# Kernel optimization log

Measured on AMD Instinct MI355X. Metric: run time of the kernel, lower is better.

## Reference

```python
import jax, jax.numpy as jnp
import numpy as np

DT = 0.01
MIN_VARIANCE = 0.01
REG_WEIGHT = 0.01
EPS = 1e-06


def setup_inputs() -> dict:
    key = jax.random.key(0)
    k1, k2, k3, k4 = jax.random.split(key, 4)
    B, T = 256, 16384
    return {
        "vel_pred": jax.random.normal(k1, (B, T, 2), dtype=jnp.float32),
        "cov_pred": jax.random.normal(k2, (B, T, 2), dtype=jnp.float32),
        "vel_gt": jax.random.normal(k3, (B, T, 2), dtype=jnp.float32),
        "pos_gt": jax.random.normal(k4, (B, T, 2), dtype=jnp.float32),
        "log_delta_v": jnp.zeros((), dtype=jnp.float32),
        "log_delta_c": jnp.zeros((), dtype=jnp.float32),
    }


def reference(vel_pred, cov_pred, vel_gt, pos_gt, log_delta_v, log_delta_c):
    # Sequential loop pos[t] = pos[t-1] + vel_pred[t-1]*dt, pos[0] = vel_pred[0]*dt
    # == dt * (vel_pred[:, 0:1] + exclusive_cumsum_T(vel_pred))  -- a parallel scan.
    excl = jnp.concatenate(
        [jnp.zeros_like(vel_pred[:, :1]), jnp.cumsum(vel_pred[:, :-1], axis=1)], axis=1
    )
    pos_pred = (vel_pred[:, :1] + excl) * DT  # [B, T, 2]

    lv_p = jnp.mean((pos_pred - pos_gt) ** 2)
    lv_e = jnp.mean((vel_pred - vel_gt) ** 2)
    lv_total = lv_p + lv_e

    sigma = jnp.clip(jnp.exp(cov_pred), MIN_VARIANCE, None)  # [B, T, 2] diag cov
    inv_sigma = 1.0 / sigma
    diff = vel_gt - vel_pred
    mahal = jnp.sum(inv_sigma * diff ** 2, axis=-1)  # [B, T]
    log_det = jnp.log(sigma[..., 0] * sigma[..., 1] + EPS)
    lc_total = 0.5 * jnp.mean(mahal + log_det)

    delta_v = jnp.exp(log_delta_v)
    delta_c = jnp.exp(log_delta_c)
    total_loss = (
        lv_total / (2.0 * delta_v ** 2)
        + lc_total / (2.0 * delta_c ** 2)
        + log_delta_v
        + log_delta_c
    )
    reg = jnp.mean(jnp.sum(inv_sigma, axis=-1))
    total_loss = total_loss + REG_WEIGHT * reg
    return total_loss
```

## Files before the change

kernel.cpp:

```cpp
#include <hip/hip_runtime.h>

static constexpr int B_ = 256;
static constexpr int T_ = 16384;
static constexpr int TPB = 1024;
static constexpr int F4_ROW = T_ * 2 / 4;
static constexpr int F4_THR = F4_ROW / TPB;

static constexpr float DTc    = 0.01f;
static constexpr float MINVAR = 0.01f;
static constexpr float EPSc   = 1e-6f;


__device__ __forceinline__ float waveReduce(float v) {
#pragma unroll
  for (int d = 32; d > 0; d >>= 1) v += __shfl_down(v, d, 64);
  return v;
}
__device__ __forceinline__ double waveReduceD(double v) {
#pragma unroll
  for (int d = 32; d > 0; d >>= 1) v += __shfl_down(v, d, 64);
  return v;
}

__global__ __launch_bounds__(TPB) void fusedKern(
    const float4* __restrict__ vel, const float4* __restrict__ cov,
    const float4* __restrict__ vgt, const float4* __restrict__ pgt,
    float* __restrict__ pPos, float* __restrict__ pLve,
    float* __restrict__ pLc,  float* __restrict__ pReg) {
  const int b = blockIdx.x;
  const int tid = threadIdx.x;
  const int lane = tid & 63, wid = tid >> 6;
  const int tbase = b * F4_ROW + tid * F4_THR;

  float4 v[F4_THR];
#pragma unroll
  for (int j = 0; j < F4_THR; ++j) v[j] = vel[tbase + j];

  float ex[F4_THR], ey[F4_THR];
  float vx[F4_THR], vy[F4_THR];
  float tx = 0.f, ty = 0.f;
#pragma unroll
  for (int j = 0; j < F4_THR; ++j) {
    ex[j] = tx; ey[j] = ty;
    vx[j] = v[j].x; vy[j] = v[j].y;
    tx += v[j].x + v[j].z;
    ty += v[j].y + v[j].w;
  }

  float lve = 0.f, lc = 0.f, reg = 0.f;
#pragma unroll
  for (int j = 0; j < F4_THR; ++j) {
    float4 c = cov[tbase + j];
    float4 g = vgt[tbase + j];
    {
      float dx = g.x - v[j].x, dy = g.y - v[j].y;
      float sqx = dx * dx, sqy = dy * dy;
      lve += sqx + sqy;
      float sx = fmaxf(__expf(c.x), MINVAR);
      float sy = fmaxf(__expf(c.y), MINVAR);
      float ixv = 1.0f / sx, iyv = 1.0f / sy;
      lc += ixv * sqx + iyv * sqy + __logf(sx * sy + EPSc);
      reg += ixv + iyv;
    }
    {
      float dx = g.z - v[j].z, dy = g.w - v[j].w;
      float sqx = dx * dx, sqy = dy * dy;
      lve += sqx + sqy;
      float sx = fmaxf(__expf(c.z), MINVAR);
      float sy = fmaxf(__expf(c.w), MINVAR);
      float ixv = 1.0f / sx, iyv = 1.0f / sy;
      lc += ixv * sqx + iyv * sqy + __logf(sx * sy + EPSc);
      reg += ixv + iyv;
    }
  }

  float sx = tx, sy = ty;
#pragma unroll
  for (int d = 1; d < 64; d <<= 1) {
    float ux = __shfl_up(sx, (unsigned)d, 64);
    float uy = __shfl_up(sy, (unsigned)d, 64);
    if (lane >= d) { sx += ux; sy += uy; }
  }
  const float wxx = sx - tx, wxy = sy - ty;

  __shared__ float2 wt[16];
  __shared__ float  sh[4][16];
  if (lane == 63) wt[wid] = make_float2(sx, sy);
  __syncthreads();

  float ax = (lane < 16) ? wt[lane].x : 0.f;
  float ay = (lane < 16) ? wt[lane].y : 0.f;
  float iax = ax, iay = ay;
#pragma unroll
  for (int d = 1; d < 16; d <<= 1) {
    float ux = __shfl_up(iax, (unsigned)d, 64);
    float uy = __shfl_up(iay, (unsigned)d, 64);
    if (lane >= d) { iax += ux; iay += uy; }
  }
  const float bx0 = __shfl(iax - ax, wid, 64);
  const float by0 = __shfl(iay - ay, wid, 64);

  const float2 v0 = ((const float2*)vel)[b * T_];

  float apos = 0.f;
#pragma unroll
  for (int j = 0; j < F4_THR; ++j) {
    float4 q = pgt[tbase + j];
    float px0 = bx0 + wxx + ex[j];
    float py0 = by0 + wxy + ey[j];
    float px = DTc * (v0.x + px0), py = DTc * (v0.y + py0);
    float e0 = px - q.x, e1 = py - q.y;
    apos += e0 * e0 + e1 * e1;
    px = DTc * (v0.x + px0 + vx[j]); py = DTc * (v0.y + py0 + vy[j]);
    e0 = px - q.z; e1 = py - q.w;
    apos += e0 * e0 + e1 * e1;
  }

  float r0 = waveReduce(apos);
  float r1 = waveReduce(lve);
  float r2 = waveReduce(lc);
  float r3 = waveReduce(reg);
  if (lane == 0) { sh[0][wid] = r0; sh[1][wid] = r1; sh[2][wid] = r2; sh[3][wid] = r3; }
  __syncthreads();
  if (tid == 0) {
    float t0 = 0.f, t1 = 0.f, t2 = 0.f, t3 = 0.f;
#pragma unroll
    for (int w = 0; w < 16; ++w) { t0 += sh[0][w]; t1 += sh[1][w]; t2 += sh[2][w]; t3 += sh[3][w]; }
    pPos[b] = t0; pLve[b] = t1; pLc[b] = t2; pReg[b] = t3;
  }
}

__global__ __launch_bounds__(256) void kernC(
    const float* __restrict__ pPos, const float* __restrict__ pLve,
    const float* __restrict__ pLc,  const float* __restrict__ pReg,
    const float* __restrict__ pldv, const float* __restrict__ pldc,
    float* __restrict__ out) {
  const int tid = threadIdx.x;
  const int lane = tid & 63, wid = tid >> 6;
  double a0 = (double)pPos[tid];
  double a1 = (double)pLve[tid];
  double a2 = (double)pLc[tid];
  double a3 = (double)pReg[tid];
  a0 = waveReduceD(a0);
  a1 = waveReduceD(a1);
  a2 = waveReduceD(a2);
  a3 = waveReduceD(a3);
  __shared__ double sh[4][4];
  if (lane == 0) { sh[0][wid] = a0; sh[1][wid] = a1; sh[2][wid] = a2; sh[3][wid] = a3; }
  __syncthreads();
  if (tid == 0) {
    double pos_sq = sh[0][0] + sh[0][1] + sh[0][2] + sh[0][3];
    double vel_sq = sh[1][0] + sh[1][1] + sh[1][2] + sh[1][3];
    double lcs    = sh[2][0] + sh[2][1] + sh[2][2] + sh[2][3];
    double regs   = sh[3][0] + sh[3][1] + sh[3][2] + sh[3][3];
    const double NBT2 = (double)B_ * (double)T_ * 2.0;
    const double NBT  = (double)B_ * (double)T_;
    double lv  = (pos_sq + vel_sq) / NBT2;
    double lc  = 0.5 * lcs / NBT;
    double reg = regs / NBT;
    double ldv = (double)pldv[0], ldc = (double)pldc[0];
    double total = lv / (2.0 * exp(2.0 * ldv)) + lc / (2.0 * exp(2.0 * ldc))
                 + ldv + ldc + 0.01 * reg;
    out[0] = (float)total;
  }
}

extern "C" void kernel_launch(void* const* d_in, const int* in_sizes, int n_in,
                              void* d_out, int out_size, void* d_ws, size_t ws_size,
                              hipStream_t stream) {
  const float4* vel = (const float4*)d_in[0];
  const float4* cov = (const float4*)d_in[1];
  const float4* vgt = (const float4*)d_in[2];
  const float4* pgt = (const float4*)d_in[3];
  const float* ldv = (const float*)d_in[4];
  const float* ldc = (const float*)d_in[5];

  char* ws = (char*)d_ws;
  float* pPos = (float*)ws;
  float* pLve = (float*)(ws + 1024);
  float* pLc  = (float*)(ws + 2048);
  float* pReg = (float*)(ws + 3072);

  fusedKern<<<B_, TPB, 0, stream>>>(vel, cov, vgt, pgt, pPos, pLve, pLc, pReg);
  kernC<<<1, 256, 0, stream>>>(pPos, pLve, pLc, pReg, ldv, ldc, (float*)d_out);
}
```

Before: 166.0 us.

## Split each row into segments and fix up the position loss algebraically

Each row of the time dimension is split into 8 segments, each handled by its own 256-thread block, so the launch grows from 256 to 2048 blocks for better occupancy and latency hiding. The prefix offset between segments is not known inside a block, so each block stores the sum of squared errors plus their linear sums. The second kernel then rebuilds the exact squared error from these using the expansion (e+dt*C)^2. All four input loads are also issued up front to raise memory-level parallelism. The cost is more registers per thread, a larger finalize step, and float cancellation risk in the algebraic correction.

```diff
diff --git a/kernel.cpp b/kernel.cpp
--- a/kernel.cpp
+++ b/kernel.cpp
@@ -2,9 +2,13 @@
 
 static constexpr int B_ = 256;
 static constexpr int T_ = 16384;
-static constexpr int TPB = 1024;
+static constexpr int THREADS = 256;
+static constexpr int SEG_T = 2048;
+static constexpr int NSEG = T_ / SEG_T;
+static constexpr int NBLK = B_ * NSEG;
 static constexpr int F4_ROW = T_ * 2 / 4;
-static constexpr int F4_THR = F4_ROW / TPB;
+static constexpr int F4_SEG = SEG_T * 2 / 4;
+static constexpr int F4_THR = F4_SEG / THREADS;
 
 static constexpr float DTc    = 0.01f;
 static constexpr float MINVAR = 0.01f;
@@ -22,56 +26,35 @@
   return v;
 }
 
-__global__ __launch_bounds__(TPB) void fusedKern(
+__global__ __launch_bounds__(THREADS) void kern1(
     const float4* __restrict__ vel, const float4* __restrict__ cov,
     const float4* __restrict__ vgt, const float4* __restrict__ pgt,
-    float* __restrict__ pPos, float* __restrict__ pLve,
-    float* __restrict__ pLc,  float* __restrict__ pReg) {
-  const int b = blockIdx.x;
+    float2* __restrict__ segsum, float* __restrict__ se2,
+    float* __restrict__ sex, float* __restrict__ sey,
+    float* __restrict__ pLve, float* __restrict__ pLc, float* __restrict__ pReg) {
+  const int bid = blockIdx.x;
+  const int b = bid >> 3, s = bid & (NSEG - 1);
   const int tid = threadIdx.x;
   const int lane = tid & 63, wid = tid >> 6;
-  const int tbase = b * F4_ROW + tid * F4_THR;
-
-  float4 v[F4_THR];
+  const int tbase = b * F4_ROW + s * F4_SEG + tid * F4_THR;
+
+  float4 v[F4_THR], c[F4_THR], g[F4_THR], q[F4_THR];
 #pragma unroll
   for (int j = 0; j < F4_THR; ++j) v[j] = vel[tbase + j];
+#pragma unroll
+  for (int j = 0; j < F4_THR; ++j) c[j] = cov[tbase + j];
+#pragma unroll
+  for (int j = 0; j < F4_THR; ++j) g[j] = vgt[tbase + j];
+#pragma unroll
+  for (int j = 0; j < F4_THR; ++j) q[j] = pgt[tbase + j];
 
   float ex[F4_THR], ey[F4_THR];
-  float vx[F4_THR], vy[F4_THR];
   float tx = 0.f, ty = 0.f;
 #pragma unroll
   for (int j = 0; j < F4_THR; ++j) {
     ex[j] = tx; ey[j] = ty;
-    vx[j] = v[j].x; vy[j] = v[j].y;
     tx += v[j].x + v[j].z;
     ty += v[j].y + v[j].w;
-  }
-
-  float lve = 0.f, lc = 0.f, reg = 0.f;
-#pragma unroll
-  for (int j = 0; j < F4_THR; ++j) {
-    float4 c = cov[tbase + j];
-    float4 g = vgt[tbase + j];
-    {
-      float dx = g.x - v[j].x, dy = g.y - v[j].y;
-      float sqx = dx * dx, sqy = dy * dy;
-      lve += sqx + sqy;
-      float sx = fmaxf(__expf(c.x), MINVAR);
-      float sy = fmaxf(__expf(c.y), MINVAR);
-      float ixv = 1.0f / sx, iyv = 1.0f / sy;
-      lc += ixv * sqx + iyv * sqy + __logf(sx * sy + EPSc);
-      reg += ixv + iyv;
-    }
-    {
-      float dx = g.z - v[j].z, dy = g.w - v[j].w;
-      float sqx = dx * dx, sqy = dy * dy;
-      lve += sqx + sqy;
-      float sx = fmaxf(__expf(c.z), MINVAR);
-      float sy = fmaxf(__expf(c.w), MINVAR);
-      float ixv = 1.0f / sx, iyv = 1.0f / sy;
-      lc += ixv * sqx + iyv * sqy + __logf(sx * sy + EPSc);
-      reg += ixv + iyv;
-    }
   }
 
   float sx = tx, sy = ty;
@@ -81,72 +64,114 @@
     float uy = __shfl_up(sy, (unsigned)d, 64);
     if (lane >= d) { sx += ux; sy += uy; }
   }
-  const float wxx = sx - tx, wxy = sy - ty;
-
-  __shared__ float2 wt[16];
-  __shared__ float  sh[4][16];
+  const float wexx = sx - tx, wexy = sy - ty;
+
+  __shared__ float2 wt[4];
   if (lane == 63) wt[wid] = make_float2(sx, sy);
   __syncthreads();
 
-  float ax = (lane < 16) ? wt[lane].x : 0.f;
-  float ay = (lane < 16) ? wt[lane].y : 0.f;
-  float iax = ax, iay = ay;
-#pragma unroll
-  for (int d = 1; d < 16; d <<= 1) {
-    float ux = __shfl_up(iax, (unsigned)d, 64);
-    float uy = __shfl_up(iay, (unsigned)d, 64);
-    if (lane >= d) { iax += ux; iay += uy; }
-  }
-  const float bx0 = __shfl(iax - ax, wid, 64);
-  const float by0 = __shfl(iay - ay, wid, 64);
+  float offx = wexx, offy = wexy;
+  float segx = 0.f, segy = 0.f;
+#pragma unroll
+  for (int w = 0; w < 4; ++w) {
+    float2 t = wt[w];
+    if (w < wid) { offx += t.x; offy += t.y; }
+    segx += t.x; segy += t.y;
+  }
 
   const float2 v0 = ((const float2*)vel)[b * T_];
 
-  float apos = 0.f;
+  float ase2 = 0.f, asex = 0.f, asey = 0.f;
 #pragma unroll
   for (int j = 0; j < F4_THR; ++j) {
-    float4 q = pgt[tbase + j];
-    float px0 = bx0 + wxx + ex[j];
-    float py0 = by0 + wxy + ey[j];
-    float px = DTc * (v0.x + px0), py = DTc * (v0.y + py0);
-    float e0 = px - q.x, e1 = py - q.y;
-    apos += e0 * e0 + e1 * e1;
-    px = DTc * (v0.x + px0 + vx[j]); py = DTc * (v0.y + py0 + vy[j]);
-    e0 = px - q.z; e1 = py - q.w;
-    apos += e0 * e0 + e1 * e1;
-  }
-
-  float r0 = waveReduce(apos);
-  float r1 = waveReduce(lve);
-  float r2 = waveReduce(lc);
-  float r3 = waveReduce(reg);
-  if (lane == 0) { sh[0][wid] = r0; sh[1][wid] = r1; sh[2][wid] = r2; sh[3][wid] = r3; }
+    float px0 = offx + ex[j], py0 = offy + ey[j];
+    float e0x = DTc * (v0.x + px0) - q[j].x;
+    float e0y = DTc * (v0.y + py0) - q[j].y;
+    float e1x = DTc * (v0.x + px0 + v[j].x) - q[j].z;
+    float e1y = DTc * (v0.y + py0 + v[j].y) - q[j].w;
+    ase2 += e0x * e0x + e0y * e0y + e1x * e1x + e1y * e1y;
+    asex += e0x + e1x;
+    asey += e0y + e1y;
+  }
+
+  float lve = 0.f, lc = 0.f, reg = 0.f;
+#pragma unroll
+  for (int j = 0; j < F4_THR; ++j) {
+    {
+      float dx = g[j].x - v[j].x, dy = g[j].y - v[j].y;
+      float sqx = dx * dx, sqy = dy * dy;
+      lve += sqx + sqy;
+      float s0 = fmaxf(__expf(c[j].x), MINVAR);
+      float s1 = fmaxf(__expf(c[j].y), MINVAR);
+      float i0 = 1.0f / s0, i1 = 1.0f / s1;
+      lc += i0 * sqx + i1 * sqy + __logf(s0 * s1 + EPSc);
+      reg += i0 + i1;
+    }
+    {
+      float dx = g[j].z - v[j].z, dy = g[j].w - v[j].w;
+      float sqx = dx * dx, sqy = dy * dy;
+      lve += sqx + sqy;
+      float s0 = fmaxf(__expf(c[j].z), MINVAR);
+      float s1 = fmaxf(__expf(c[j].w), MINVAR);
+      float i0 = 1.0f / s0, i1 = 1.0f / s1;
+      lc += i0 * sqx + i1 * sqy + __logf(s0 * s1 + EPSc);
+      reg += i0 + i1;
+    }
+  }
+
+  float r0 = waveReduce(ase2);
+  float r1 = waveReduce(asex);
+  float r2 = waveReduce(asey);
+  float r3 = waveReduce(lve);
+  float r4 = waveReduce(lc);
+  float r5 = waveReduce(reg);
+  __shared__ float sh[6][4];
+  if (lane == 0) { sh[0][wid] = r0; sh[1][wid] = r1; sh[2][wid] = r2;
+                   sh[3][wid] = r3; sh[4][wid] = r4; sh[5][wid] = r5; }
   __syncthreads();
   if (tid == 0) {
-    float t0 = 0.f, t1 = 0.f, t2 = 0.f, t3 = 0.f;
-#pragma unroll
-    for (int w = 0; w < 16; ++w) { t0 += sh[0][w]; t1 += sh[1][w]; t2 += sh[2][w]; t3 += sh[3][w]; }
-    pPos[b] = t0; pLve[b] = t1; pLc[b] = t2; pReg[b] = t3;
-  }
-}
-
-__global__ __launch_bounds__(256) void kernC(
-    const float* __restrict__ pPos, const float* __restrict__ pLve,
-    const float* __restrict__ pLc,  const float* __restrict__ pReg,
+    segsum[bid] = make_float2(segx, segy);
+    se2[bid] = sh[0][0] + sh[0][1] + sh[0][2] + sh[0][3];
+    sex[bid] = sh[1][0] + sh[1][1] + sh[1][2] + sh[1][3];
+    sey[bid] = sh[2][0] + sh[2][1] + sh[2][2] + sh[2][3];
+    pLve[bid] = sh[3][0] + sh[3][1] + sh[3][2] + sh[3][3];
+    pLc [bid] = sh[4][0] + sh[4][1] + sh[4][2] + sh[4][3];
+    pReg[bid] = sh[5][0] + sh[5][1] + sh[5][2] + sh[5][3];
+  }
+}
+
+__global__ __launch_bounds__(THREADS) void kern2(
+    const float2* __restrict__ segsum, const float* __restrict__ se2,
+    const float* __restrict__ sex, const float* __restrict__ sey,
+    const float* __restrict__ pLve, const float* __restrict__ pLc,
+    const float* __restrict__ pReg,
     const float* __restrict__ pldv, const float* __restrict__ pldc,
     float* __restrict__ out) {
   const int tid = threadIdx.x;
   const int lane = tid & 63, wid = tid >> 6;
-  double a0 = (double)pPos[tid];
-  double a1 = (double)pLve[tid];
-  double a2 = (double)pLc[tid];
-  double a3 = (double)pReg[tid];
-  a0 = waveReduceD(a0);
-  a1 = waveReduceD(a1);
-  a2 = waveReduceD(a2);
-  a3 = waveReduceD(a3);
+
+  double posAcc = 0.0, lveAcc = 0.0, lcAcc = 0.0, regAcc = 0.0;
+  double Cx = 0.0, Cy = 0.0;
+  const double dDT = (double)DTc;
+#pragma unroll
+  for (int s = 0; s < NSEG; ++s) {
+    int idx = tid * NSEG + s;
+    float2 ss = segsum[idx];
+    posAcc += (double)se2[idx]
+            + 2.0 * dDT * (Cx * (double)sex[idx] + Cy * (double)sey[idx])
+            + (double)SEG_T * dDT * dDT * (Cx * Cx + Cy * Cy);
+    lveAcc += (double)pLve[idx];
+    lcAcc  += (double)pLc[idx];
+    regAcc += (double)pReg[idx];
+    Cx += (double)ss.x; Cy += (double)ss.y;
+  }
+
+  posAcc = waveReduceD(posAcc);
+  lveAcc = waveReduceD(lveAcc);
+  lcAcc  = waveReduceD(lcAcc);
+  regAcc = waveReduceD(regAcc);
   __shared__ double sh[4][4];
-  if (lane == 0) { sh[0][wid] = a0; sh[1][wid] = a1; sh[2][wid] = a2; sh[3][wid] = a3; }
+  if (lane == 0) { sh[0][wid] = posAcc; sh[1][wid] = lveAcc; sh[2][wid] = lcAcc; sh[3][wid] = regAcc; }
   __syncthreads();
   if (tid == 0) {
     double pos_sq = sh[0][0] + sh[0][1] + sh[0][2] + sh[0][3];
@@ -176,11 +201,16 @@
   const float* ldc = (const float*)d_in[5];
 
   char* ws = (char*)d_ws;
-  float* pPos = (float*)ws;
-  float* pLve = (float*)(ws + 1024);
-  float* pLc  = (float*)(ws + 2048);
-  float* pReg = (float*)(ws + 3072);
-
-  fusedKern<<<B_, TPB, 0, stream>>>(vel, cov, vgt, pgt, pPos, pLve, pLc, pReg);
-  kernC<<<1, 256, 0, stream>>>(pPos, pLve, pLc, pReg, ldv, ldc, (float*)d_out);
-}
+  float2* segsum = (float2*)ws;
+  float* se2  = (float*)(ws + 16 * 1024);
+  float* sex  = (float*)(ws + 24 * 1024);
+  float* sey  = (float*)(ws + 32 * 1024);
+  float* pLve = (float*)(ws + 40 * 1024);
+  float* pLc  = (float*)(ws + 48 * 1024);
+  float* pReg = (float*)(ws + 56 * 1024);
+
+  kern1<<<NBLK, THREADS, 0, stream>>>(vel, cov, vgt, pgt, segsum, se2, sex, sey,
+                                      pLve, pLc, pReg);
+  kern2<<<1, THREADS, 0, stream>>>(segsum, se2, sex, sey, pLve, pLc, pReg,
+                                   ldv, ldc, (float*)d_out);
+}
```

New measurement: 155.3 us. -6.5%, faster.
